# Optimization experiments

Measured on AMD Instinct MI355X. Metric: run time of the kernel, lower is better.

Reference implementation:

```python
import jax, jax.numpy as jnp
import numpy as np

SPATIAL_SCALE = 0.25
N, C, H, W = 8, 256, 128, 128
P = 100000
IMG = 512.0  # image-space extent (H / spatial_scale)


def setup_inputs() -> dict:
    key = jax.random.key(0)
    k1, k2, k3, k4 = jax.random.split(key, 4)
    features = jax.random.normal(k1, (N, C, H, W), dtype=jnp.float32)
    batch_idx = jax.random.randint(k2, (P,), 0, N).astype(jnp.float32)
    xy = jax.random.uniform(k3, (P, 2), dtype=jnp.float32) * IMG
    rois = jnp.concatenate([batch_idx[:, None], xy], axis=1)  # [P,3]: (b, x, y)
    return {"features": features, "rois": rois}


def _interp(features, rois, spatial_scale):
    n, c, h, w = features.shape
    b = rois[:, 0].astype(jnp.int32)
    x = rois[:, 1] * spatial_scale
    y = rois[:, 2] * spatial_scale
    # RoIAlign-style bilinear interpolation with boundary handling
    valid = (y >= -1.0) & (y <= h) & (x >= -1.0) & (x <= w)
    y = jnp.maximum(y, 0.0)
    x = jnp.maximum(x, 0.0)
    y_low = jnp.floor(y).astype(jnp.int32)
    x_low = jnp.floor(x).astype(jnp.int32)
    y_at_edge = y_low >= h - 1
    x_at_edge = x_low >= w - 1
    y_low = jnp.minimum(y_low, h - 1)
    x_low = jnp.minimum(x_low, w - 1)
    y_high = jnp.where(y_at_edge, y_low, y_low + 1)
    x_high = jnp.where(x_at_edge, x_low, x_low + 1)
    y = jnp.where(y_at_edge, y_low.astype(y.dtype), y)
    x = jnp.where(x_at_edge, x_low.astype(x.dtype), x)
    ly = y - y_low
    lx = x - x_low
    hy = 1.0 - ly
    hx = 1.0 - lx
    w1 = (hy * hx)[:, None]  # [P,1]
    w2 = (hy * lx)[:, None]
    w3 = (ly * hx)[:, None]
    w4 = (ly * lx)[:, None]
    # fancy-index gather: [P, C] per corner
    v1 = features[b, :, y_low, x_low]
    v2 = features[b, :, y_low, x_high]
    v3 = features[b, :, y_high, x_low]
    v4 = features[b, :, y_high, x_high]
    out = w1 * v1 + w2 * v2 + w3 * v3 + w4 * v4  # [P, C]
    return jnp.where(valid[:, None], out, 0.0)


def reference(features, rois):
    return _interp(features, rois, SPATIAL_SCALE)
```

## Files before the change

### kernel.cpp

```cpp
#include <hip/hip_runtime.h>

#define SCALE   0.25f
#define NBATCH  8
#define CCH     256
#define HH      128
#define WW      128
#define NBUCK   (NBATCH * HH)
#define CG      16
#define NCG     (CCH / CG)
#define CAP     160
#define PADC    257


__global__ void k_bin(const float* __restrict__ rois, int* __restrict__ cnt,
                      int4* __restrict__ slots, int P) {
    int p = blockIdx.x * 256 + threadIdx.x;
    if (p >= P) return;
    float fb = rois[3 * p];
    float fx = rois[3 * p + 1] * SCALE;
    float fy = rois[3 * p + 2] * SCALE;
    int b = (int)fb;
    bool valid = (fy >= -1.0f) && (fy <= (float)HH) &&
                 (fx >= -1.0f) && (fx <= (float)WW);
    float y = fmaxf(fy, 0.0f);
    float x = fmaxf(fx, 0.0f);
    int ylo = (int)floorf(y);
    int xlo = (int)floorf(x);
    float yf = y, xf = x;
    int xhi;
    if (ylo >= HH - 1) { ylo = HH - 1; yf = (float)ylo; }
    if (xlo >= WW - 1) { xlo = WW - 1; xhi = WW - 1; xf = (float)xlo; }
    else               { xhi = xlo + 1; }
    float ly = yf - (float)ylo;
    float lx = xf - (float)xlo;
    int flo = ((xlo & 3) << 5) | (xlo >> 2);
    int fhi = ((xhi & 3) << 5) | (xhi >> 2);
    unsigned pk = (unsigned)flo | ((unsigned)fhi << 8) | (valid ? 0u : 0x80000000u);
    int bk = b * HH + ylo;
    int pos = atomicAdd(&cnt[bk], 1);
    if (pos < CAP)
        slots[bk * CAP + pos] =
            make_int4(p, (int)pk, __float_as_int(lx), __float_as_int(ly));
}

__global__ __launch_bounds__(256, 8) void k_main(
    const float* __restrict__ feat, const int4* __restrict__ slots,
    const int* __restrict__ cnt_arr, float* __restrict__ out)
{
    const int bk = blockIdx.x >> 4;
    const int cg = blockIdx.x & 15;
    const int cnt = min(cnt_arr[bk], CAP);
    if (cnt == 0) return;
    const int b  = bk >> 7;
    const int yl = bk & 127;
    const int yh = min(yl + 1, HH - 1);

    __shared__ float lds[CG * PADC];

    const int t = threadIdx.x;
    const float* base = feat + (size_t)(b * CCH + cg * CG) * (HH * WW);
#pragma unroll
    for (int k = 0; k < 4; ++k) {
        int id  = k * 256 + t;
        int x4  = id & 31;
        int row = (id >> 5) & 1;
        int c   = id >> 6;
        int y   = row ? yh : yl;
        float4 v = *(const float4*)(base + (size_t)c * (HH * WW) + y * WW + x4 * 4);
        float* d = &lds[c * PADC + row * WW + x4];
        d[0]  = v.x;
        d[32] = v.y;
        d[64] = v.z;
        d[96] = v.w;
    }
    __syncthreads();

    const int wv   = t >> 6;
    const int lane = t & 63;
    const int sub  = lane >> 3;
    const int c0   = (lane & 7) << 1;
    const float* ldc = &lds[c0 * PADC];
    const int4* sb = slots + bk * CAP;

    for (int ii = wv * 8; ii < cnt; ii += 32) {
        int i = ii + sub;
        bool act = (i < cnt);
        int4 r = sb[act ? i : cnt - 1];
        unsigned pk = (unsigned)r.y;
        float lx = __int_as_float(r.z);
        float ly = __int_as_float(r.w);
        float s  = ((int)pk < 0) ? 0.0f : 1.0f;
        float hy = (1.0f - ly) * s;
        float lys = ly * s;
        float hx = 1.0f - lx;
        float w1 = hy * hx, w2 = hy * lx, w3 = lys * hx, w4 = lys * lx;
        int flo = pk & 255;
        int fhi = (pk >> 8) & 255;

        float v1 = ldc[flo], v2 = ldc[fhi];
        float v3 = ldc[WW + flo], v4 = ldc[WW + fhi];
        float o0 = w1 * v1 + w2 * v2 + w3 * v3 + w4 * v4;
        v1 = ldc[PADC + flo]; v2 = ldc[PADC + fhi];
        v3 = ldc[PADC + WW + flo]; v4 = ldc[PADC + WW + fhi];
        float o1 = w1 * v1 + w2 * v2 + w3 * v3 + w4 * v4;

        if (act)
            *(float2*)(out + (size_t)r.x * CCH + cg * CG + c0) = make_float2(o0, o1);
    }
}

extern "C" void kernel_launch(void* const* d_in, const int* in_sizes, int n_in,
                              void* d_out, int out_size, void* d_ws, size_t ws_size,
                              hipStream_t stream) {
    const float* feat = (const float*)d_in[0];
    const float* rois = (const float*)d_in[1];
    float* out = (float*)d_out;
    const int P = in_sizes[1] / 3;

    int*  cnt   = (int*)d_ws;
    int4* slots = (int4*)((char*)d_ws + NBUCK * sizeof(int));

    hipMemsetAsync(cnt, 0, NBUCK * sizeof(int), stream);
    const int pb = (P + 255) / 256;
    k_bin<<<pb, 256, 0, stream>>>(rois, cnt, slots, P);
    k_main<<<NBUCK * NCG, 256, 0, stream>>>(feat, slots, cnt, out);
}
```

Baseline: 266.2 us.

## Aggregate binning via shared histograms and widen main blocks to 32 channels

The binning kernel now builds a per-block shared-memory histogram over 4096 rois and issues one global atomic per bucket to reserve slot ranges, replacing one global atomic per roi. The main kernel handles 32 channels per block with 512 threads, so each slot record is read once for twice as many channels, and blocks are reordered so consecutive blocks cover different buckets of the same channel group. The exchange is fewer, larger blocks with more LDS each, which can lower occupancy, and slot order inside a bucket changes, which does not affect results.

Measured after the change: 238.0 us. -10.6%, faster.

```diff
diff --git a/kernel.cpp b/kernel.cpp
--- a/kernel.cpp
+++ b/kernel.cpp
@@ -6,49 +6,76 @@
 #define HH      128
 #define WW      128
 #define NBUCK   (NBATCH * HH)
-#define CG      16
+#define CG      32
 #define NCG     (CCH / CG)
 #define CAP     160
 #define PADC    257
+#define BIN_PASS 4
 
 
-__global__ void k_bin(const float* __restrict__ rois, int* __restrict__ cnt,
-                      int4* __restrict__ slots, int P) {
-    int p = blockIdx.x * 256 + threadIdx.x;
-    if (p >= P) return;
-    float fb = rois[3 * p];
-    float fx = rois[3 * p + 1] * SCALE;
-    float fy = rois[3 * p + 2] * SCALE;
-    int b = (int)fb;
-    bool valid = (fy >= -1.0f) && (fy <= (float)HH) &&
-                 (fx >= -1.0f) && (fx <= (float)WW);
-    float y = fmaxf(fy, 0.0f);
-    float x = fmaxf(fx, 0.0f);
-    int ylo = (int)floorf(y);
-    int xlo = (int)floorf(x);
-    float yf = y, xf = x;
-    int xhi;
-    if (ylo >= HH - 1) { ylo = HH - 1; yf = (float)ylo; }
-    if (xlo >= WW - 1) { xlo = WW - 1; xhi = WW - 1; xf = (float)xlo; }
-    else               { xhi = xlo + 1; }
-    float ly = yf - (float)ylo;
-    float lx = xf - (float)xlo;
-    int flo = ((xlo & 3) << 5) | (xlo >> 2);
-    int fhi = ((xhi & 3) << 5) | (xhi >> 2);
-    unsigned pk = (unsigned)flo | ((unsigned)fhi << 8) | (valid ? 0u : 0x80000000u);
-    int bk = b * HH + ylo;
-    int pos = atomicAdd(&cnt[bk], 1);
-    if (pos < CAP)
-        slots[bk * CAP + pos] =
-            make_int4(p, (int)pk, __float_as_int(lx), __float_as_int(ly));
+__global__ __launch_bounds__(1024) void k_bin(
+    const float* __restrict__ rois, int* __restrict__ cnt,
+    int4* __restrict__ slots, int P)
+{
+    __shared__ int lhist[NBUCK];
+    __shared__ int lbase[NBUCK];
+    const int t = threadIdx.x;
+    lhist[t] = 0;
+    __syncthreads();
+
+    int  mybk[BIN_PASS], mypos[BIN_PASS];
+    int4 myrec[BIN_PASS];
+#pragma unroll
+    for (int s = 0; s < BIN_PASS; ++s) {
+        int p = (blockIdx.x * BIN_PASS + s) * 1024 + t;
+        mybk[s] = -1;
+        if (p < P) {
+            float fb = rois[3 * p];
+            float fx = rois[3 * p + 1] * SCALE;
+            float fy = rois[3 * p + 2] * SCALE;
+            int b = (int)fb;
+            bool valid = (fy >= -1.0f) && (fy <= (float)HH) &&
+                         (fx >= -1.0f) && (fx <= (float)WW);
+            float y = fmaxf(fy, 0.0f);
+            float x = fmaxf(fx, 0.0f);
+            int ylo = (int)floorf(y);
+            int xlo = (int)floorf(x);
+            float yf = y, xf = x;
+            int xhi;
+            if (ylo >= HH - 1) { ylo = HH - 1; yf = (float)ylo; }
+            if (xlo >= WW - 1) { xlo = WW - 1; xhi = WW - 1; xf = (float)xlo; }
+            else               { xhi = xlo + 1; }
+            float ly = yf - (float)ylo;
+            float lx = xf - (float)xlo;
+            int flo = ((xlo & 3) << 5) | (xlo >> 2);
+            int fhi = ((xhi & 3) << 5) | (xhi >> 2);
+            unsigned pk = (unsigned)flo | ((unsigned)fhi << 8) | (valid ? 0u : 0x80000000u);
+            int bk = b * HH + ylo;
+            mybk[s]  = bk;
+            mypos[s] = atomicAdd(&lhist[bk], 1);
+            myrec[s] = make_int4(p, (int)pk, __float_as_int(lx), __float_as_int(ly));
+        }
+    }
+    __syncthreads();
+    int h = lhist[t];
+    lbase[t] = h ? atomicAdd(&cnt[t], h) : 0;
+    __syncthreads();
+#pragma unroll
+    for (int s = 0; s < BIN_PASS; ++s) {
+        int bk = mybk[s];
+        if (bk >= 0) {
+            int idx = lbase[bk] + mypos[s];
+            if (idx < CAP) slots[bk * CAP + idx] = myrec[s];
+        }
+    }
 }
 
-__global__ __launch_bounds__(256, 8) void k_main(
+__global__ __launch_bounds__(512, 8) void k_main(
     const float* __restrict__ feat, const int4* __restrict__ slots,
     const int* __restrict__ cnt_arr, float* __restrict__ out)
 {
-    const int bk = blockIdx.x >> 4;
-    const int cg = blockIdx.x & 15;
+    const int bk = blockIdx.x & (NBUCK - 1);
+    const int cg = blockIdx.x >> 10;
     const int cnt = min(cnt_arr[bk], CAP);
     if (cnt == 0) return;
     const int b  = bk >> 7;
@@ -61,7 +88,7 @@
     const float* base = feat + (size_t)(b * CCH + cg * CG) * (HH * WW);
 #pragma unroll
     for (int k = 0; k < 4; ++k) {
-        int id  = k * 256 + t;
+        int id  = k * 512 + t;
         int x4  = id & 31;
         int row = (id >> 5) & 1;
         int c   = id >> 6;
@@ -77,12 +104,12 @@
 
     const int wv   = t >> 6;
     const int lane = t & 63;
-    const int sub  = lane >> 3;
-    const int c0   = (lane & 7) << 1;
+    const int sub  = lane >> 4;
+    const int c0   = (lane & 15) << 1;
     const float* ldc = &lds[c0 * PADC];
     const int4* sb = slots + bk * CAP;
 
-    for (int ii = wv * 8; ii < cnt; ii += 32) {
+    for (int ii = wv * 4; ii < cnt; ii += 32) {
         int i = ii + sub;
         bool act = (i < cnt);
         int4 r = sb[act ? i : cnt - 1];
@@ -121,7 +148,7 @@
     int4* slots = (int4*)((char*)d_ws + NBUCK * sizeof(int));
 
     hipMemsetAsync(cnt, 0, NBUCK * sizeof(int), stream);
-    const int pb = (P + 255) / 256;
-    k_bin<<<pb, 256, 0, stream>>>(rois, cnt, slots, P);
-    k_main<<<NBUCK * NCG, 256, 0, stream>>>(feat, slots, cnt, out);
+    const int bb = (P + BIN_PASS * 1024 - 1) / (BIN_PASS * 1024);
+    k_bin<<<bb, 1024, 0, stream>>>(rois, cnt, slots, P);
+    k_main<<<NCG * NBUCK, 512, 0, stream>>>(feat, slots, cnt, out);
 }
```
